# Performance work log

Measured on AMD Instinct MI355X. Metric: run time of the kernel, lower is better.

Reference implementation:

```python
import jax, jax.numpy as jnp
import numpy as np
from jax.ops import segment_sum

N_NODES = 100000
IN_C, HID_C, OUT_C = 128, 128, 64
N_EDGES = 1600000


def gcn_conv(x, row, col, dinv, W, b):
    # PyG GCNConv: symmetric normalization with self-loops.
    # h = X W; out[c] = sum_{(r,c) in E} dinv[r]*dinv[c]*h[r] + dinv[v]^2*h[v] + b
    h = x @ W  # [N, F_out]
    norm = dinv[row] * dinv[col]  # [E]
    agg = segment_sum(h[row] * norm[:, None], col, num_segments=x.shape[0])
    agg = agg + h * (dinv * dinv)[:, None]  # self-loop contribution
    return agg + b


def setup_inputs() -> dict:
    key = jax.random.key(0)
    k1, k2, k3, k4, k5, k6 = jax.random.split(key, 6)
    x = jax.random.normal(k1, (N_NODES, IN_C), dtype=jnp.float32)
    edge_index = jax.random.randint(k2, (2, N_EDGES), 0, N_NODES, dtype=jnp.int64)
    # Glorot-style init for GCN weights, zero bias (as in PyG GCNConv)
    W1 = jax.random.normal(k3, (IN_C, HID_C), dtype=jnp.float32) / np.sqrt(IN_C)
    b1 = jnp.zeros((HID_C,), dtype=jnp.float32)
    W2 = jax.random.normal(k4, (HID_C, OUT_C), dtype=jnp.float32) / np.sqrt(HID_C)
    b2 = jnp.zeros((OUT_C,), dtype=jnp.float32)
    return {"x": x, "edge_index": edge_index, "W1": W1, "b1": b1, "W2": W2, "b2": b2}


def reference(x, edge_index, W1, b1, W2, b2):
    row, col = edge_index[0], edge_index[1]
    n = x.shape[0]
    # degree counts include self-loop (+1)
    deg = segment_sum(jnp.ones_like(col, dtype=x.dtype), col, num_segments=n) + 1.0
    dinv = jax.lax.rsqrt(deg)
    h = gcn_conv(x, row, col, dinv, W1, b1)
    h = jax.nn.relu(h)
    # dropout is identity in eval mode (get_embedding runs model.eval())
    out = gcn_conv(h, row, col, dinv, W2, b2)
    return out
```

## Files before the change

kernel.cpp:

```cpp
#include <hip/hip_runtime.h>
#include <math.h>


#define BS 256
#define EPB 4096
#define BK_SHIFT 9

typedef __attribute__((ext_vector_type(8))) short bf16x8;
typedef __attribute__((ext_vector_type(4))) float f32x4;
typedef __attribute__((ext_vector_type(4))) unsigned u32x4;

union FragU {
    bf16x8 v;
    unsigned u[4];
};

__device__ __forceinline__ unsigned pack_bf16x2(float a, float b) {
    unsigned ua = __float_as_uint(a);
    unsigned ub = __float_as_uint(b);
    ua = (ua + 0x7fffu + ((ua >> 16) & 1u)) >> 16;
    ub = (ub + 0x7fffu + ((ub >> 16) & 1u)) >> 16;
    return ua | (ub << 16);
}

__device__ __forceinline__ ushort bf16_rte(float a) {
    unsigned ua = __float_as_uint(a);
    return (ushort)((ua + 0x7fffu + ((ua >> 16) & 1u)) >> 16);
}

__device__ __forceinline__ float bf_lo(unsigned u) { return __uint_as_float(u << 16); }
__device__ __forceinline__ float bf_hi(unsigned u) { return __uint_as_float(u & 0xffff0000u); }

__global__ __launch_bounds__(BS) void p1_hist_kernel(const int* __restrict__ col,
                                                     int* __restrict__ countsT,
                                                     int E, int NBUCK, int NBLK) {
    __shared__ int h[256];
    int tid = threadIdx.x;
    h[tid] = 0;
    __syncthreads();
    int e0 = blockIdx.x * EPB;
    int e1 = min(e0 + EPB, E);
    for (int i = e0 + tid; i < e1; i += BS) atomicAdd(&h[col[i] >> BK_SHIFT], 1);
    __syncthreads();
    for (int b = tid; b < NBUCK; b += BS) countsT[b * NBLK + blockIdx.x] = h[b];
}

__global__ __launch_bounds__(BS) void scan_block_kernel(const int* __restrict__ in,
                                                        int* __restrict__ exc,
                                                        int* __restrict__ bsum, int N) {
    __shared__ int s[BS];
    int tid = threadIdx.x;
    int i = blockIdx.x * BS + tid;
    int v = (i < N) ? in[i] : 0;
    s[tid] = v;
    __syncthreads();
    for (int off = 1; off < BS; off <<= 1) {
        int t = (tid >= off) ? s[tid - off] : 0;
        __syncthreads();
        s[tid] += t;
        __syncthreads();
    }
    if (i < N) exc[i] = s[tid] - v;
    if (tid == BS - 1) bsum[blockIdx.x] = s[BS - 1];
}

__global__ __launch_bounds__(512) void scan_bsum_kernel(const int* __restrict__ bsum,
                                                        int* __restrict__ boff, int NB) {
    __shared__ int s[512];
    int tid = threadIdx.x;
    int v = (tid < NB) ? bsum[tid] : 0;
    s[tid] = v;
    __syncthreads();
    for (int off = 1; off < 512; off <<= 1) {
        int t = (tid >= off) ? s[tid - off] : 0;
        __syncthreads();
        s[tid] += t;
        __syncthreads();
    }
    if (tid < NB) boff[tid] = s[tid] - v;
}

__global__ __launch_bounds__(BS) void add_off_kernel(int* __restrict__ exc,
                                                     const int* __restrict__ boff, int N) {
    int i = blockIdx.x * BS + threadIdx.x;
    if (i < N) exc[i] += boff[blockIdx.x];
}

__global__ __launch_bounds__(BS) void p2_scatter_kernel(const int* __restrict__ row,
                                                        const int* __restrict__ col,
                                                        const int* __restrict__ baseT,
                                                        uint2* __restrict__ pairs,
                                                        int E, int NBUCK, int NBLK) {
    __shared__ int cur[256];
    int tid = threadIdx.x;
    for (int b = tid; b < NBUCK; b += BS) cur[b] = baseT[b * NBLK + blockIdx.x];
    __syncthreads();
    int e0 = blockIdx.x * EPB;
    int e1 = min(e0 + EPB, E);
    for (int i = e0 + tid; i < e1; i += BS) {
        int c = col[i];
        int r = row[i];
        int pos = atomicAdd(&cur[c >> BK_SHIFT], 1);
        pairs[pos] = make_uint2((unsigned)r, (unsigned)c);
    }
}

__global__ __launch_bounds__(BS) void p3_build_kernel(const uint2* __restrict__ pairs,
                                                      const int* __restrict__ baseT,
                                                      int* __restrict__ off_g,
                                                      int* __restrict__ deg_g,
                                                      float* __restrict__ dinv,
                                                      int* __restrict__ src,
                                                      int E, int n, int NBUCK, int NBLK) {
    __shared__ int cnt[512];
    __shared__ int scn[512];
    __shared__ int a256[256];
    int tid = threadIdx.x;
    int b = blockIdx.x;
    int s = baseT[b * NBLK];
    int eEnd = (b == NBUCK - 1) ? E : baseT[(b + 1) * NBLK];

    cnt[tid] = 0;
    cnt[tid + 256] = 0;
    __syncthreads();
    for (int i = s + tid; i < eEnd; i += BS) {
        uint2 p = pairs[i];
        atomicAdd(&cnt[p.y & 511], 1);
    }
    __syncthreads();
    int pairsum = cnt[2 * tid] + cnt[2 * tid + 1];
    a256[tid] = pairsum;
    __syncthreads();
    for (int off = 1; off < 256; off <<= 1) {
        int t = (tid >= off) ? a256[tid - off] : 0;
        __syncthreads();
        a256[tid] += t;
        __syncthreads();
    }
    int exc = a256[tid] - pairsum;
    scn[2 * tid] = exc;
    scn[2 * tid + 1] = exc + cnt[2 * tid];
    __syncthreads();
#pragma unroll
    for (int l = tid; l < 512; l += BS) {
        int node = (b << BK_SHIFT) + l;
        if (node < n) {
            off_g[node] = s + scn[l];
            deg_g[node] = cnt[l];
            dinv[node] = rsqrtf((float)(cnt[l] + 1));
        }
    }
    __syncthreads();
#pragma unroll
    for (int l = tid; l < 512; l += BS) scn[l] += s;
    __syncthreads();
    for (int i = s + tid; i < eEnd; i += BS) {
        uint2 p = pairs[i];
        int pos = atomicAdd(&scn[p.y & 511], 1);
        src[pos] = (int)p.x;
    }
}

__global__ __launch_bounds__(BS) void wprep_kernel(const float* __restrict__ W1,
                                                   const float* __restrict__ W2,
                                                   ushort* __restrict__ wt1,
                                                   ushort* __restrict__ wt2) {
    int t = blockIdx.x * BS + threadIdx.x;
    if (t < 128 * 128) {
        int nn = t >> 7, k = t & 127;
        wt1[t] = bf16_rte(W1[k * 128 + nn]);
    }
    if (t < 64 * 128) {
        int nn = t >> 7, k = t & 127;
        wt2[t] = bf16_rte(W2[k * 64 + nn]);
    }
}

template <int NCH, bool IN_BF16>
__global__ __launch_bounds__(BS) void gemm_mfma_kernel(const void* __restrict__ Ain,
                                                       const ushort* __restrict__ WT,
                                                       const float* __restrict__ dinv,
                                                       unsigned* __restrict__ G, int n) {
    constexpr int NT = NCH / 16;
    constexpr int KP = 136;
    __shared__ ushort wlds[NCH * KP];

    int tid = threadIdx.x;
    for (int c = tid; c < NCH * 16; c += BS) {
        int nr = c >> 4, q16 = c & 15;
        *(uint4*)(wlds + nr * KP + q16 * 8) = ((const uint4*)WT)[c];
    }
    __syncthreads();

    int lane = tid & 63, wv = tid >> 6;
    int ml = lane & 15, quad = lane >> 4;
    int m = blockIdx.x * 64 + wv * 16 + ml;

    FragU b[4];
    if (m < n) {
        if (IN_BF16) {
#pragma unroll
            for (int ks = 0; ks < 4; ++ks) {
                uint4 t = ((const uint4*)Ain)[(size_t)m * 16 + ks * 4 + quad];
                b[ks].u[0] = t.x; b[ks].u[1] = t.y; b[ks].u[2] = t.z; b[ks].u[3] = t.w;
            }
        } else {
            const float4* A = (const float4*)Ain + (size_t)m * 32;
#pragma unroll
            for (int ks = 0; ks < 4; ++ks) {
                float4 p0 = A[ks * 8 + quad * 2];
                float4 p1 = A[ks * 8 + quad * 2 + 1];
                b[ks].u[0] = pack_bf16x2(p0.x, p0.y);
                b[ks].u[1] = pack_bf16x2(p0.z, p0.w);
                b[ks].u[2] = pack_bf16x2(p1.x, p1.y);
                b[ks].u[3] = pack_bf16x2(p1.z, p1.w);
            }
        }
    } else {
#pragma unroll
        for (int ks = 0; ks < 4; ++ks) {
            b[ks].u[0] = 0; b[ks].u[1] = 0; b[ks].u[2] = 0; b[ks].u[3] = 0;
        }
    }

    f32x4 acc[NT];
#pragma unroll
    for (int nt = 0; nt < NT; ++nt) {
        acc[nt][0] = 0.f; acc[nt][1] = 0.f; acc[nt][2] = 0.f; acc[nt][3] = 0.f;
    }

#pragma unroll
    for (int nt = 0; nt < NT; ++nt) {
#pragma unroll
        for (int ks = 0; ks < 4; ++ks) {
            bf16x8 a = *(const bf16x8*)(wlds + (nt * 16 + ml) * KP + ks * 32 + quad * 8);
            acc[nt] = __builtin_amdgcn_mfma_f32_16x16x32_bf16(a, b[ks].v, acc[nt], 0, 0, 0);
        }
    }

    if (m < n) {
        float dv = dinv[m];
        unsigned* grow = G + (size_t)m * (NCH / 2);
#pragma unroll
        for (int nt = 0; nt < NT; ++nt) {
            uint2 o;
            o.x = pack_bf16x2(acc[nt][0] * dv, acc[nt][1] * dv);
            o.y = pack_bf16x2(acc[nt][2] * dv, acc[nt][3] * dv);
            *(uint2*)(grow + nt * 8 + quad * 2) = o;
        }
    }
}

template <int C, bool RELU, bool OUT_BF16>
__global__ __launch_bounds__(BS) void agg_kernel(const unsigned* __restrict__ G,
                                                 const int* __restrict__ edge_off,
                                                 const int* __restrict__ cnt,
                                                 const int* __restrict__ src,
                                                 const float* __restrict__ dinv,
                                                 const float* __restrict__ bias,
                                                 void* __restrict__ out, int n) {
    constexpr int Gp = C / 8;
    constexpr int NPB = BS / Gp;
    int lane = threadIdx.x & (Gp - 1);
    int li = threadIdx.x / Gp;
    int node = blockIdx.x * NPB + li;
    if (node >= n) return;

    const uint4* G4 = (const uint4*)G;
    float acc[8];
    {
        uint4 sv = G4[(size_t)node * Gp + lane];
        acc[0] = bf_lo(sv.x); acc[1] = bf_hi(sv.x);
        acc[2] = bf_lo(sv.y); acc[3] = bf_hi(sv.y);
        acc[4] = bf_lo(sv.z); acc[5] = bf_hi(sv.z);
        acc[6] = bf_lo(sv.w); acc[7] = bf_hi(sv.w);
    }
    const int* sp = src + edge_off[node];
    int deg = cnt[node];

#define ACCUM(v)                                                               \
    acc[0] += bf_lo(v.x); acc[1] += bf_hi(v.x);                                \
    acc[2] += bf_lo(v.y); acc[3] += bf_hi(v.y);                                \
    acc[4] += bf_lo(v.z); acc[5] += bf_hi(v.z);                                \
    acc[6] += bf_lo(v.w); acc[7] += bf_hi(v.w);

    int i = 0;
    for (; i + Gp <= deg; i += Gp) {
        int myi = __builtin_nontemporal_load(sp + i + lane);
#pragma unroll
        for (int h = 0; h < Gp / 8; ++h) {
            uint4 v[8];
#pragma unroll
            for (int u = 0; u < 8; ++u) {
                int s = __shfl(myi, h * 8 + u, Gp);
                v[u] = G4[(size_t)s * Gp + lane];
            }
#pragma unroll
            for (int u = 0; u < 8; ++u) { ACCUM(v[u]) }
        }
    }
    int rem = deg - i;
    if (rem > 0) {
        int myi = (lane < rem) ? __builtin_nontemporal_load(sp + i + lane) : 0;
        int j = 0;
        if (Gp == 16 && rem >= 8) {
            uint4 v[8];
#pragma unroll
            for (int u = 0; u < 8; ++u) {
                int s = __shfl(myi, u, Gp);
                v[u] = G4[(size_t)s * Gp + lane];
            }
#pragma unroll
            for (int u = 0; u < 8; ++u) { ACCUM(v[u]) }
            j = 8;
        }
        if (rem - j >= 4) {
            uint4 v[4];
#pragma unroll
            for (int u = 0; u < 4; ++u) {
                int s = __shfl(myi, j + u, Gp);
                v[u] = G4[(size_t)s * Gp + lane];
            }
#pragma unroll
            for (int u = 0; u < 4; ++u) { ACCUM(v[u]) }
            j += 4;
        }
        if (rem - j >= 2) {
            uint4 v0, v1;
            {
                int s0 = __shfl(myi, j, Gp);
                int s1 = __shfl(myi, j + 1, Gp);
                v0 = G4[(size_t)s0 * Gp + lane];
                v1 = G4[(size_t)s1 * Gp + lane];
            }
            ACCUM(v0) ACCUM(v1)
            j += 2;
        }
        if (rem - j >= 1) {
            int s0 = __shfl(myi, j, Gp);
            uint4 v0 = G4[(size_t)s0 * Gp + lane];
            ACCUM(v0)
        }
    }
#undef ACCUM

    float dv = dinv[node];
    const float4* b4 = (const float4*)bias;
    float4 bl = b4[2 * lane + 0], bh = b4[2 * lane + 1];
    float o0x = acc[0] * dv + bl.x, o0y = acc[1] * dv + bl.y;
    float o0z = acc[2] * dv + bl.z, o0w = acc[3] * dv + bl.w;
    float o1x = acc[4] * dv + bh.x, o1y = acc[5] * dv + bh.y;
    float o1z = acc[6] * dv + bh.z, o1w = acc[7] * dv + bh.w;
    if (RELU) {
        o0x = fmaxf(o0x, 0.f); o0y = fmaxf(o0y, 0.f);
        o0z = fmaxf(o0z, 0.f); o0w = fmaxf(o0w, 0.f);
        o1x = fmaxf(o1x, 0.f); o1y = fmaxf(o1y, 0.f);
        o1z = fmaxf(o1z, 0.f); o1w = fmaxf(o1w, 0.f);
    }
    if (OUT_BF16) {
        u32x4 ov;
        ov.x = pack_bf16x2(o0x, o0y);
        ov.y = pack_bf16x2(o0z, o0w);
        ov.z = pack_bf16x2(o1x, o1y);
        ov.w = pack_bf16x2(o1z, o1w);
        __builtin_nontemporal_store(ov, (u32x4*)out + (size_t)node * Gp + lane);
    } else {
        f32x4* orow = (f32x4*)((float*)out + (size_t)node * C);
        f32x4 o0; o0.x = o0x; o0.y = o0y; o0.z = o0z; o0.w = o0w;
        f32x4 o1; o1.x = o1x; o1.y = o1y; o1.z = o1z; o1.w = o1w;
        __builtin_nontemporal_store(o0, orow + 2 * lane + 0);
        __builtin_nontemporal_store(o1, orow + 2 * lane + 1);
    }
}

extern "C" void kernel_launch(void* const* d_in, const int* in_sizes, int n_in,
                              void* d_out, int out_size, void* d_ws, size_t ws_size,
                              hipStream_t stream) {
    const float* x  = (const float*)d_in[0];
    const int*   ei = (const int*)d_in[1];
    const float* W1 = (const float*)d_in[2];
    const float* b1 = (const float*)d_in[3];
    const float* W2 = (const float*)d_in[4];
    const float* b2 = (const float*)d_in[5];

    const int IN_C = 128, HID_C = 128;
    int n = in_sizes[0] / IN_C;
    int E = in_sizes[1] / 2;
    const int* row = ei;
    const int* col = ei + E;

    int NBUCK = (n + 511) >> BK_SHIFT;
    int NBLK = (E + EPB - 1) / EPB;
    int M = NBUCK * NBLK;
    int NBS = (M + BS - 1) / BS;

    char* w = (char*)d_ws;
    auto alloc = [&](size_t bytes) {
        void* p = (void*)w;
        w += (bytes + 255) & ~(size_t)255;
        return p;
    };
    int*      countsT = (int*)alloc((size_t)M * 4);
    int*      baseT   = (int*)alloc((size_t)M * 4);
    int*      bsum    = (int*)alloc((size_t)NBS * 4);
    int*      boff    = (int*)alloc((size_t)NBS * 4);
    uint2*    pairs   = (uint2*)alloc((size_t)E * 8);
    int*      src     = (int*)alloc((size_t)E * 4);
    int*      off     = (int*)alloc((size_t)n * 4);
    int*      deg     = (int*)alloc((size_t)n * 4);
    float*    dinv    = (float*)alloc((size_t)n * 4);
    ushort*   wt1     = (ushort*)alloc(128 * 128 * 2);
    ushort*   wt2     = (ushort*)alloc(64 * 128 * 2);
    unsigned* g       = (unsigned*)alloc((size_t)n * HID_C * 2);
    unsigned* h1b     = (unsigned*)alloc((size_t)n * HID_C * 2);

    wprep_kernel<<<64, BS, 0, stream>>>(W1, W2, wt1, wt2);

    p1_hist_kernel<<<NBLK, BS, 0, stream>>>(col, countsT, E, NBUCK, NBLK);
    scan_block_kernel<<<NBS, BS, 0, stream>>>(countsT, baseT, bsum, M);
    scan_bsum_kernel<<<1, 512, 0, stream>>>(bsum, boff, NBS);
    add_off_kernel<<<NBS, BS, 0, stream>>>(baseT, boff, M);
    p2_scatter_kernel<<<NBLK, BS, 0, stream>>>(row, col, baseT, pairs, E, NBUCK, NBLK);
    p3_build_kernel<<<NBUCK, BS, 0, stream>>>(pairs, baseT, off, deg, dinv, src,
                                              E, n, NBUCK, NBLK);

    int gridM = (n + 63) / 64;

    gemm_mfma_kernel<128, false><<<gridM, BS, 0, stream>>>(x, wt1, dinv, g, n);
    agg_kernel<128, true, true><<<(n + 15) / 16, BS, 0, stream>>>(g, off, deg, src,
                                                                  dinv, b1, h1b, n);

    gemm_mfma_kernel<64, true><<<gridM, BS, 0, stream>>>(h1b, wt2, dinv, g, n);
    agg_kernel<64, false, false><<<(n + 31) / 32, BS, 0, stream>>>(g, off, deg, src,
                                                                   dinv, b2, d_out, n);
}
```

Measured before the change: 276.4 us.

## Sort nodes by degree within block and prefetch next edge-index chunk

Measured after the change: 286.5 us. 3.7% more time.

```diff
diff --git a/kernel.cpp b/kernel.cpp
--- a/kernel.cpp
+++ b/kernel.cpp
@@ -261,10 +261,38 @@
                                                  void* __restrict__ out, int n) {
     constexpr int Gp = C / 8;
     constexpr int NPB = BS / Gp;
-    int lane = threadIdx.x & (Gp - 1);
-    int li = threadIdx.x / Gp;
-    int node = blockIdx.x * NPB + li;
+
+    __shared__ int sdeg[NPB], soff[NPB], sprm[NPB];
+    __shared__ float sdnv[NPB];
+    int tid = threadIdx.x;
+    if (tid < NPB) {
+        int nd = blockIdx.x * NPB + tid;
+        bool ok = nd < n;
+        sdeg[tid] = ok ? cnt[nd] : -1;
+        soff[tid] = ok ? edge_off[nd] : 0;
+        sdnv[tid] = ok ? dinv[nd] : 0.f;
+    }
+    __syncthreads();
+    if (tid < NPB) {
+        int d = sdeg[tid];
+        int r = 0;
+#pragma unroll
+        for (int j = 0; j < NPB; ++j) {
+            int dj = sdeg[j];
+            r += (int)((dj > d) || (dj == d && j < tid));
+        }
+        sprm[r] = tid;
+    }
+    __syncthreads();
+
+    int lane = tid & (Gp - 1);
+    int li = tid / Gp;
+    int sl = sprm[li];
+    int node = blockIdx.x * NPB + sl;
     if (node >= n) return;
+    int deg = sdeg[sl];
+    const int* sp = src + soff[sl];
+    float dv = sdnv[sl];
 
     const uint4* G4 = (const uint4*)G;
     float acc[8];
@@ -275,8 +303,6 @@
         acc[4] = bf_lo(sv.z); acc[5] = bf_hi(sv.z);
         acc[6] = bf_lo(sv.w); acc[7] = bf_hi(sv.w);
     }
-    const int* sp = src + edge_off[node];
-    int deg = cnt[node];
 
 #define ACCUM(v)                                                               \
     acc[0] += bf_lo(v.x); acc[1] += bf_hi(v.x);                                \
@@ -284,67 +310,88 @@
     acc[4] += bf_lo(v.z); acc[5] += bf_hi(v.z);                                \
     acc[6] += bf_lo(v.w); acc[7] += bf_hi(v.w);
 
+    int myi0, myi1 = 0;
+    if constexpr (Gp == 16) {
+        myi0 = __builtin_nontemporal_load(sp + lane);
+    } else {
+        myi0 = __builtin_nontemporal_load(sp + lane);
+        myi1 = __builtin_nontemporal_load(sp + 8 + lane);
+    }
+
     int i = 0;
-    for (; i + Gp <= deg; i += Gp) {
-        int myi = __builtin_nontemporal_load(sp + i + lane);
-#pragma unroll
-        for (int h = 0; h < Gp / 8; ++h) {
-            uint4 v[8];
-#pragma unroll
-            for (int u = 0; u < 8; ++u) {
-                int s = __shfl(myi, h * 8 + u, Gp);
-                v[u] = G4[(size_t)s * Gp + lane];
-            }
-#pragma unroll
-            for (int u = 0; u < 8; ++u) { ACCUM(v[u]) }
-        }
-    }
+    for (; i + 16 <= deg; i += 16) {
+        int nx0, nx1 = 0;
+        if constexpr (Gp == 16) {
+            nx0 = __builtin_nontemporal_load(sp + i + 16 + lane);
+        } else {
+            nx0 = __builtin_nontemporal_load(sp + i + 16 + lane);
+            nx1 = __builtin_nontemporal_load(sp + i + 24 + lane);
+        }
+        uint4 v[8];
+#pragma unroll
+        for (int u = 0; u < 8; ++u) {
+            int s = __shfl(myi0, u, Gp);
+            v[u] = G4[(size_t)s * Gp + lane];
+        }
+#pragma unroll
+        for (int u = 0; u < 8; ++u) { ACCUM(v[u]) }
+#pragma unroll
+        for (int u = 0; u < 8; ++u) {
+            int s = (Gp == 16) ? __shfl(myi0, 8 + u, Gp) : __shfl(myi1, u, Gp);
+            v[u] = G4[(size_t)s * Gp + lane];
+        }
+#pragma unroll
+        for (int u = 0; u < 8; ++u) { ACCUM(v[u]) }
+        myi0 = nx0;
+        if constexpr (Gp == 8) myi1 = nx1;
+    }
+
     int rem = deg - i;
-    if (rem > 0) {
-        int myi = (lane < rem) ? __builtin_nontemporal_load(sp + i + lane) : 0;
-        int j = 0;
-        if (Gp == 16 && rem >= 8) {
-            uint4 v[8];
-#pragma unroll
-            for (int u = 0; u < 8; ++u) {
-                int s = __shfl(myi, u, Gp);
-                v[u] = G4[(size_t)s * Gp + lane];
-            }
-#pragma unroll
-            for (int u = 0; u < 8; ++u) { ACCUM(v[u]) }
-            j = 8;
-        }
-        if (rem - j >= 4) {
-            uint4 v[4];
-#pragma unroll
-            for (int u = 0; u < 4; ++u) {
-                int s = __shfl(myi, j + u, Gp);
-                v[u] = G4[(size_t)s * Gp + lane];
-            }
-#pragma unroll
-            for (int u = 0; u < 4; ++u) { ACCUM(v[u]) }
-            j += 4;
-        }
-        if (rem - j >= 2) {
-            uint4 v0, v1;
-            {
-                int s0 = __shfl(myi, j, Gp);
-                int s1 = __shfl(myi, j + 1, Gp);
-                v0 = G4[(size_t)s0 * Gp + lane];
-                v1 = G4[(size_t)s1 * Gp + lane];
-            }
-            ACCUM(v0) ACCUM(v1)
-            j += 2;
-        }
-        if (rem - j >= 1) {
-            int s0 = __shfl(myi, j, Gp);
-            uint4 v0 = G4[(size_t)s0 * Gp + lane];
-            ACCUM(v0)
-        }
+    if (rem >= 8) {
+        uint4 v[8];
+#pragma unroll
+        for (int u = 0; u < 8; ++u) {
+            int s = __shfl(myi0, u, Gp);
+            v[u] = G4[(size_t)s * Gp + lane];
+        }
+#pragma unroll
+        for (int u = 0; u < 8; ++u) { ACCUM(v[u]) }
+    }
+    int rest, jb;
+    if constexpr (Gp == 8) {
+        rest = (rem >= 8) ? myi1 : myi0;
+        jb = 0;
+    } else {
+        rest = myi0;
+        jb = (rem >= 8) ? 8 : 0;
+    }
+    int r2 = rem & 7;
+    if (r2 >= 4) {
+        uint4 v[4];
+#pragma unroll
+        for (int u = 0; u < 4; ++u) {
+            int s = __shfl(rest, jb + u, Gp);
+            v[u] = G4[(size_t)s * Gp + lane];
+        }
+#pragma unroll
+        for (int u = 0; u < 4; ++u) { ACCUM(v[u]) }
+        jb += 4;
+    }
+    if (r2 & 2) {
+        int s0 = __shfl(rest, jb, Gp);
+        int s1 = __shfl(rest, jb + 1, Gp);
+        uint4 v0 = G4[(size_t)s0 * Gp + lane];
+        uint4 v1 = G4[(size_t)s1 * Gp + lane];
+        ACCUM(v0) ACCUM(v1)
+        jb += 2;
+    }
+    if (r2 & 1) {
+        int s0 = __shfl(rest, jb, Gp);
+        uint4 v0 = G4[(size_t)s0 * Gp + lane];
+        ACCUM(v0)
     }
 #undef ACCUM
 
-    float dv = dinv[node];
     const float4* b4 = (const float4*)bias;
     float4 bl = b4[2 * lane + 0], bh = b4[2 * lane + 1];
     float o0x = acc[0] * dv + bl.x, o0y = acc[1] * dv + bl.y;
```

## Fold scan offset into consumers and prefetch edge indices in 64-wide aggregation

Applied to the files above, without the earlier changes.

New measurement: 455.4 us. +64.8%, slower.

```diff
diff --git a/kernel.cpp b/kernel.cpp
--- a/kernel.cpp
+++ b/kernel.cpp
@@ -80,20 +80,18 @@
     if (tid < NB) boff[tid] = s[tid] - v;
 }
 
-__global__ __launch_bounds__(BS) void add_off_kernel(int* __restrict__ exc,
-                                                     const int* __restrict__ boff, int N) {
-    int i = blockIdx.x * BS + threadIdx.x;
-    if (i < N) exc[i] += boff[blockIdx.x];
-}
-
 __global__ __launch_bounds__(BS) void p2_scatter_kernel(const int* __restrict__ row,
                                                         const int* __restrict__ col,
                                                         const int* __restrict__ baseT,
+                                                        const int* __restrict__ boff,
                                                         uint2* __restrict__ pairs,
                                                         int E, int NBUCK, int NBLK) {
     __shared__ int cur[256];
     int tid = threadIdx.x;
-    for (int b = tid; b < NBUCK; b += BS) cur[b] = baseT[b * NBLK + blockIdx.x];
+    for (int b = tid; b < NBUCK; b += BS) {
+        int idx = b * NBLK + blockIdx.x;
+        cur[b] = baseT[idx] + boff[idx >> 8];
+    }
     __syncthreads();
     int e0 = blockIdx.x * EPB;
     int e1 = min(e0 + EPB, E);
@@ -107,6 +105,7 @@
 
 __global__ __launch_bounds__(BS) void p3_build_kernel(const uint2* __restrict__ pairs,
                                                       const int* __restrict__ baseT,
+                                                      const int* __restrict__ boff,
                                                       int* __restrict__ off_g,
                                                       int* __restrict__ deg_g,
                                                       float* __restrict__ dinv,
@@ -117,8 +116,15 @@
     __shared__ int a256[256];
     int tid = threadIdx.x;
     int b = blockIdx.x;
-    int s = baseT[b * NBLK];
-    int eEnd = (b == NBUCK - 1) ? E : baseT[(b + 1) * NBLK];
+    int i0 = b * NBLK;
+    int s = baseT[i0] + boff[i0 >> 8];
+    int eEnd;
+    if (b == NBUCK - 1) {
+        eEnd = E;
+    } else {
+        int i1 = (b + 1) * NBLK;
+        eEnd = baseT[i1] + boff[i1 >> 8];
+    }
 
     cnt[tid] = 0;
     cnt[tid + 256] = 0;
@@ -252,13 +258,13 @@
 }
 
 template <int C, bool RELU, bool OUT_BF16>
-__global__ __launch_bounds__(BS) void agg_kernel(const unsigned* __restrict__ G,
-                                                 const int* __restrict__ edge_off,
-                                                 const int* __restrict__ cnt,
-                                                 const int* __restrict__ src,
-                                                 const float* __restrict__ dinv,
-                                                 const float* __restrict__ bias,
-                                                 void* __restrict__ out, int n) {
+__global__ __launch_bounds__(BS, 8) void agg_kernel(const unsigned* __restrict__ G,
+                                                    const int* __restrict__ edge_off,
+                                                    const int* __restrict__ cnt,
+                                                    const int* __restrict__ src,
+                                                    const float* __restrict__ dinv,
+                                                    const float* __restrict__ bias,
+                                                    void* __restrict__ out, int n) {
     constexpr int Gp = C / 8;
     constexpr int NPB = BS / Gp;
     int lane = threadIdx.x & (Gp - 1);
@@ -284,60 +290,122 @@
     acc[4] += bf_lo(v.z); acc[5] += bf_hi(v.z);                                \
     acc[6] += bf_lo(v.w); acc[7] += bf_hi(v.w);
 
-    int i = 0;
-    for (; i + Gp <= deg; i += Gp) {
-        int myi = __builtin_nontemporal_load(sp + i + lane);
-#pragma unroll
-        for (int h = 0; h < Gp / 8; ++h) {
-            uint4 v[8];
-#pragma unroll
-            for (int u = 0; u < 8; ++u) {
-                int s = __shfl(myi, h * 8 + u, Gp);
-                v[u] = G4[(size_t)s * Gp + lane];
-            }
-#pragma unroll
-            for (int u = 0; u < 8; ++u) { ACCUM(v[u]) }
-        }
-    }
-    int rem = deg - i;
-    if (rem > 0) {
-        int myi = (lane < rem) ? __builtin_nontemporal_load(sp + i + lane) : 0;
-        int j = 0;
-        if (Gp == 16 && rem >= 8) {
-            uint4 v[8];
-#pragma unroll
-            for (int u = 0; u < 8; ++u) {
-                int s = __shfl(myi, u, Gp);
-                v[u] = G4[(size_t)s * Gp + lane];
-            }
-#pragma unroll
-            for (int u = 0; u < 8; ++u) { ACCUM(v[u]) }
-            j = 8;
-        }
-        if (rem - j >= 4) {
-            uint4 v[4];
-#pragma unroll
-            for (int u = 0; u < 4; ++u) {
-                int s = __shfl(myi, j + u, Gp);
-                v[u] = G4[(size_t)s * Gp + lane];
-            }
-#pragma unroll
-            for (int u = 0; u < 4; ++u) { ACCUM(v[u]) }
-            j += 4;
-        }
-        if (rem - j >= 2) {
-            uint4 v0, v1;
-            {
+    if constexpr (Gp == 16) {
+        int i = 0;
+        for (; i + Gp <= deg; i += Gp) {
+            int myi = __builtin_nontemporal_load(sp + i + lane);
+#pragma unroll
+            for (int h = 0; h < Gp / 8; ++h) {
+                uint4 v[8];
+#pragma unroll
+                for (int u = 0; u < 8; ++u) {
+                    int s = __shfl(myi, h * 8 + u, Gp);
+                    v[u] = G4[(size_t)s * Gp + lane];
+                }
+#pragma unroll
+                for (int u = 0; u < 8; ++u) { ACCUM(v[u]) }
+            }
+        }
+        int rem = deg - i;
+        if (rem > 0) {
+            int myi = (lane < rem) ? __builtin_nontemporal_load(sp + i + lane) : 0;
+            int j = 0;
+            if (rem >= 8) {
+                uint4 v[8];
+#pragma unroll
+                for (int u = 0; u < 8; ++u) {
+                    int s = __shfl(myi, u, Gp);
+                    v[u] = G4[(size_t)s * Gp + lane];
+                }
+#pragma unroll
+                for (int u = 0; u < 8; ++u) { ACCUM(v[u]) }
+                j = 8;
+            }
+            if (rem - j >= 4) {
+                uint4 v[4];
+#pragma unroll
+                for (int u = 0; u < 4; ++u) {
+                    int s = __shfl(myi, j + u, Gp);
+                    v[u] = G4[(size_t)s * Gp + lane];
+                }
+#pragma unroll
+                for (int u = 0; u < 4; ++u) { ACCUM(v[u]) }
+                j += 4;
+            }
+            if (rem - j >= 2) {
                 int s0 = __shfl(myi, j, Gp);
                 int s1 = __shfl(myi, j + 1, Gp);
-                v0 = G4[(size_t)s0 * Gp + lane];
-                v1 = G4[(size_t)s1 * Gp + lane];
-            }
+                uint4 v0 = G4[(size_t)s0 * Gp + lane];
+                uint4 v1 = G4[(size_t)s1 * Gp + lane];
+                ACCUM(v0) ACCUM(v1)
+                j += 2;
+            }
+            if (rem - j >= 1) {
+                int s0 = __shfl(myi, j, Gp);
+                uint4 v0 = G4[(size_t)s0 * Gp + lane];
+                ACCUM(v0)
+            }
+        }
+    } else {
+        int myi0 = __builtin_nontemporal_load(sp + lane);
+        int myi1 = __builtin_nontemporal_load(sp + 8 + lane);
+        int i = 0;
+        for (; i + 16 <= deg; i += 16) {
+            int nx0 = __builtin_nontemporal_load(sp + i + 16 + lane);
+            int nx1 = __builtin_nontemporal_load(sp + i + 24 + lane);
+            uint4 v[8];
+#pragma unroll
+            for (int u = 0; u < 8; ++u) {
+                int s = __shfl(myi0, u, Gp);
+                v[u] = G4[(size_t)s * Gp + lane];
+            }
+#pragma unroll
+            for (int u = 0; u < 8; ++u) { ACCUM(v[u]) }
+#pragma unroll
+            for (int u = 0; u < 8; ++u) {
+                int s = __shfl(myi1, u, Gp);
+                v[u] = G4[(size_t)s * Gp + lane];
+            }
+#pragma unroll
+            for (int u = 0; u < 8; ++u) { ACCUM(v[u]) }
+            myi0 = nx0;
+            myi1 = nx1;
+        }
+        int rem = deg - i;
+        if (rem >= 8) {
+            uint4 v[8];
+#pragma unroll
+            for (int u = 0; u < 8; ++u) {
+                int s = __shfl(myi0, u, Gp);
+                v[u] = G4[(size_t)s * Gp + lane];
+            }
+#pragma unroll
+            for (int u = 0; u < 8; ++u) { ACCUM(v[u]) }
+        }
+        int rest = (rem >= 8) ? myi1 : myi0;
+        int jb = 0;
+        int r2 = rem & 7;
+        if (r2 >= 4) {
+            uint4 v[4];
+#pragma unroll
+            for (int u = 0; u < 4; ++u) {
+                int s = __shfl(rest, jb + u, Gp);
+                v[u] = G4[(size_t)s * Gp + lane];
+            }
+#pragma unroll
+            for (int u = 0; u < 4; ++u) { ACCUM(v[u]) }
+            jb += 4;
+        }
+        if (r2 & 2) {
+            int s0 = __shfl(rest, jb, Gp);
+            int s1 = __shfl(rest, jb + 1, Gp);
+            uint4 v0 = G4[(size_t)s0 * Gp + lane];
+            uint4 v1 = G4[(size_t)s1 * Gp + lane];
             ACCUM(v0) ACCUM(v1)
-            j += 2;
-        }
-        if (rem - j >= 1) {
-            int s0 = __shfl(myi, j, Gp);
+            jb += 2;
+        }
+        if (r2 & 1) {
+            int s0 = __shfl(rest, jb, Gp);
             uint4 v0 = G4[(size_t)s0 * Gp + lane];
             ACCUM(v0)
         }
@@ -419,10 +487,10 @@
     p1_hist_kernel<<<NBLK, BS, 0, stream>>>(col, countsT, E, NBUCK, NBLK);
     scan_block_kernel<<<NBS, BS, 0, stream>>>(countsT, baseT, bsum, M);
     scan_bsum_kernel<<<1, 512, 0, stream>>>(bsum, boff, NBS);
-    add_off_kernel<<<NBS, BS, 0, stream>>>(baseT, boff, M);
-    p2_scatter_kernel<<<NBLK, BS, 0, stream>>>(row, col, baseT, pairs, E, NBUCK, NBLK);
-    p3_build_kernel<<<NBUCK, BS, 0, stream>>>(pairs, baseT, off, deg, dinv, src,
-                                              E, n, NBUCK, NBLK);
+    p2_scatter_kernel<<<NBLK, BS, 0, stream>>>(row, col, baseT, boff, pairs,
+                                               E, NBUCK, NBLK);
+    p3_build_kernel<<<NBUCK, BS, 0, stream>>>(pairs, baseT, boff, off, deg, dinv,
+                                              src, E, n, NBUCK, NBLK);
 
     int gridM = (n + 63) / 64;
 
```
